# Kernel optimization log

Hardware: AMD Instinct MI355X
Metric: run time of the kernel (lower is better)

Reference implementation:

```python
import jax, jax.numpy as jnp
import numpy as np

VOCAB, EMBED, HIDDEN = 32000, 256, 512
N, L = 256, 512


def setup_inputs() -> dict:
    key = jax.random.key(0)
    ks = jax.random.split(key, 6)
    X = jax.random.randint(ks[0], (N, L), 0, VOCAB)
    emb = jax.random.normal(ks[1], (VOCAB, EMBED), dtype=jnp.float32)
    # torch Linear: y = x @ W.T + b, W:(out,in)
    W_hh = jax.random.normal(ks[2], (HIDDEN, HIDDEN), dtype=jnp.float32) / np.sqrt(HIDDEN)
    b_hh = jax.random.normal(ks[3], (HIDDEN,), dtype=jnp.float32) * 0.01
    W_xh = jax.random.normal(ks[4], (HIDDEN, EMBED), dtype=jnp.float32) / np.sqrt(EMBED)
    b_xh = jax.random.normal(ks[5], (HIDDEN,), dtype=jnp.float32) * 0.01
    return {"X": X, "emb": emb, "W_hh": W_hh, "b_hh": b_hh, "W_xh": W_xh, "b_xh": b_xh}


def reference(X, emb, W_hh, b_hh, W_xh, b_xh):
    Xe = emb[X]                       # (N, L, E) embedding lookup
    # precompute input projections for all steps (parallel GEMM)
    Xproj = jnp.einsum('nle,he->nlh', Xe, W_xh) + b_xh  # (N, L, H)
    Xproj_t = jnp.swapaxes(Xproj, 0, 1)                 # (L, N, H)
    h0 = jnp.zeros((X.shape[0], W_hh.shape[0]), dtype=emb.dtype)

    def step(h, xp):
        h_new = jnp.tanh(h @ W_hh.T + b_hh + xp)
        return h_new, None

    H_last, _ = jax.lax.scan(step, h0, Xproj_t)
    return H_last
```

## Files before the change

kernel.cpp:

```cpp
#include <hip/hip_runtime.h>


typedef _Float16 f16;
typedef f16 f16x8 __attribute__((ext_vector_type(8)));
typedef float f32x4 __attribute__((ext_vector_type(4)));
typedef unsigned short u16;

union U8 { uint4 u; f16x8 h; };
union U4 { uint2 u; f16 h[4]; };

__global__ void preconv_kernel(const float* __restrict__ W, u16* __restrict__ dst,
                               int kstride, int mode) {
  int t = blockIdx.x * blockDim.x + threadIdx.x;
  int f = t >> 6, l = t & 63;
  int kt, w, nt;
  if (mode == 0)    { kt = f & 7;  nt = (f >> 3) & 3; w = f >> 5; }
  else if (f < 384) { nt = f & 3;  w = (f >> 2) & 7;  kt = f >> 5; }
  else { int g = f - 384; kt = 12 + (g & 3); nt = (g >> 2) & 3; w = g >> 4; }
  int col = w * 64 + nt * 16 + (l & 15);
  int k   = kt * 32 + (l >> 4) * 8;
  const float* src = W + (size_t)col * kstride + k;
  float4 v0 = *(const float4*)src;
  float4 v1 = *(const float4*)(src + 4);
  U8 r;
  r.h = (f16x8){(f16)v0.x, (f16)v0.y, (f16)v0.z, (f16)v0.w,
                (f16)v1.x, (f16)v1.y, (f16)v1.z, (f16)v1.w};
  *(uint4*)(dst + (size_t)f * 512 + l * 8) = r.u;
}

__global__ __launch_bounds__(512, 2) void phaseA_kernel(
    const int* __restrict__ X, const float* __restrict__ emb,
    const u16* __restrict__ Wxf, const float* __restrict__ b_hh,
    const float* __restrict__ b_xh, u16* __restrict__ xpf) {
  __shared__ f16 A[128 * 256];
  const int tid = threadIdx.x, w = tid >> 6, l = tid & 63;
  const int b = blockIdx.x, bn = b >> 6, bl = b & 63;
  const int lr = l & 15, lg = l >> 4;

  f16x8 wx[4][8];
#pragma unroll
  for (int mt = 0; mt < 4; ++mt)
#pragma unroll
    for (int kt = 0; kt < 8; ++kt) {
      U8 u; u.u = *(const uint4*)(Wxf + (size_t)((w * 4 + mt) * 8 + kt) * 512 + l * 8);
      wx[mt][kt] = u.h;
    }
  float bias[4][4];
#pragma unroll
  for (int mt = 0; mt < 4; ++mt)
#pragma unroll
    for (int r = 0; r < 4; ++r) {
      int c = w * 64 + mt * 16 + lg * 4 + r;
      bias[mt][r] = b_hh[c] + b_xh[c];
    }

  int xs[16];
  const int lseq = bl * 8 + w;
#pragma unroll
  for (int i = 0; i < 16; ++i) xs[i] = X[(bn * 16 + i) * 512 + lseq];
#pragma unroll
  for (int i = 0; i < 16; ++i) {
    float4 v = *(const float4*)(emb + (size_t)xs[i] * 256 + l * 4);
    U4 p; p.h[0] = (f16)v.x; p.h[1] = (f16)v.y; p.h[2] = (f16)v.z; p.h[3] = (f16)v.w;
    int row = w * 16 + i;
    *(uint2*)(&A[row * 256 + ((l * 4) ^ ((row & 7) << 3))]) = p.u;
  }
  __syncthreads();

#pragma unroll 1
  for (int nt = 0; nt < 8; ++nt) {
    f32x4 acc[4];
#pragma unroll
    for (int mt = 0; mt < 4; ++mt) acc[mt] = (f32x4){0.f, 0.f, 0.f, 0.f};
    const f16* Brow = &A[(nt * 16 + lr) * 256];
    const int sw = (lr & 7) << 3;
#pragma unroll
    for (int kt = 0; kt < 8; ++kt) {
      f16x8 bfr = *(const f16x8*)(Brow + ((kt * 32 + lg * 8) ^ sw));
#pragma unroll
      for (int mt = 0; mt < 4; ++mt)
        acc[mt] = __builtin_amdgcn_mfma_f32_16x16x32_f16(wx[mt][kt], bfr, acc[mt], 0, 0, 0);
    }
    const int t = bl * 8 + nt;
#pragma unroll
    for (int mt = 0; mt < 4; ++mt) {
      U4 p;
#pragma unroll
      for (int r = 0; r < 4; ++r) p.h[r] = (f16)(acc[mt][r] + bias[mt][r]);
      *(uint2*)(xpf + (size_t)t * 131072 + (w * 16 + mt * 4 + lg) * 1024
                    + (bn * 16 + lr) * 4) = p.u;
    }
  }
}

__global__ __launch_bounds__(512)
__attribute__((amdgpu_waves_per_eu(2, 2)))
void phaseB_kernel(const u16* __restrict__ Whf, const u16* __restrict__ xpf,
                   float* __restrict__ out) {
  extern __shared__ char smem[];
  f16* h0 = (f16*)smem;
  f16* h1 = (f16*)(smem + 16 * 1024);
  u16* wl = (u16*)(smem + 32 * 1024);
  const int tid = threadIdx.x, w = tid >> 6, l = tid & 63;
  const int bb = blockIdx.x;
  const int lr = l & 15, lg = l >> 4;

  f16x8 wa[12][4];
#pragma unroll
  for (int kt = 0; kt < 12; ++kt)
#pragma unroll
    for (int mt = 0; mt < 4; ++mt) {
      U8 u; u.u = *(const uint4*)(Whf + (size_t)(kt * 32 + w * 4 + mt) * 512 + l * 8);
      wa[kt][mt] = u.h;
    }
  {
    const uint4* src = (const uint4*)(Whf + (size_t)384 * 512);
    uint4* dst = (uint4*)wl;
#pragma unroll
    for (int i = 0; i < 16; ++i) dst[i * 512 + tid] = src[i * 512 + tid];
  }
  {
    float* hz = (float*)h0;
#pragma unroll
    for (int i = 0; i < 8; ++i) hz[i * 512 + tid] = 0.f;
  }
  __syncthreads();

  const u16* wt  = wl + w * 8192 + l * 8;
  const u16* xpb = xpf + (w * 16 + lg) * 1024 + (bb * 16 + lr) * 4;
  const int asw = (lr & 7) << 3;

#define RNN_STEP(HR, HW, XP)                                                     \
  do {                                                                           \
    f32x4 acc[4];                                                                \
    _Pragma("unroll")                                                            \
    for (int mt = 0; mt < 4; ++mt) acc[mt] = (f32x4){0.f, 0.f, 0.f, 0.f};        \
    _Pragma("unroll")                                                            \
    for (int kt = 0; kt < 12; ++kt) {                                            \
      f16x8 hb = *(const f16x8*)((HR) + lr * 512 + ((kt * 32 + lg * 8) ^ asw));  \
      _Pragma("unroll")                                                          \
      for (int mt = 0; mt < 4; ++mt)                                             \
        acc[mt] = __builtin_amdgcn_mfma_f32_16x16x32_f16(wa[kt][mt], hb, acc[mt], 0, 0, 0); \
    }                                                                            \
    _Pragma("unroll")                                                            \
    for (int kt = 12; kt < 16; ++kt) {                                           \
      f16x8 hb = *(const f16x8*)((HR) + lr * 512 + ((kt * 32 + lg * 8) ^ asw));  \
      _Pragma("unroll")                                                          \
      for (int mt = 0; mt < 4; ++mt) {                                           \
        U8 u; u.u = *(const uint4*)(wt + (mt * 4 + (kt - 12)) * 512);            \
        acc[mt] = __builtin_amdgcn_mfma_f32_16x16x32_f16(u.h, hb, acc[mt], 0, 0, 0); \
      }                                                                          \
    }                                                                            \
    _Pragma("unroll")                                                            \
    for (int mt = 0; mt < 4; ++mt) {                                             \
      U4 px; px.u = (XP)[mt];                                                    \
      U4 o;                                                                      \
      _Pragma("unroll")                                                          \
      for (int r = 0; r < 4; ++r) {                                              \
        float z = acc[mt][r] + (float)px.h[r];                                   \
        float e = exp2f(z * 2.885390081777927f);                                 \
        o.h[r] = (f16)(1.0f - 2.0f * __builtin_amdgcn_rcpf(e + 1.0f));           \
      }                                                                          \
      *(uint2*)((HW) + lr * 512 + ((w * 64 + mt * 16 + lg * 4) ^ asw)) = o.u;    \
    }                                                                            \
    __syncthreads();                                                             \
  } while (0)

  uint2 xpA[4], xpB[4];
#pragma unroll
  for (int mt = 0; mt < 4; ++mt) xpA[mt] = *(const uint2*)(xpb + mt * 4096);

#pragma unroll 1
  for (int tt = 0; tt < 256; ++tt) {
    const int t = tt * 2;
    {
      const u16* p = xpb + (size_t)(t + 1) * 131072;
#pragma unroll
      for (int mt = 0; mt < 4; ++mt) xpB[mt] = *(const uint2*)(p + mt * 4096);
    }
    RNN_STEP(h0, h1, xpA);
    {
      const int tn = (t + 2 < 512) ? (t + 2) : 511;
      const u16* p = xpb + (size_t)tn * 131072;
#pragma unroll
      for (int mt = 0; mt < 4; ++mt) xpA[mt] = *(const uint2*)(p + mt * 4096);
    }
    RNN_STEP(h1, h0, xpB);
  }
#undef RNN_STEP

#pragma unroll
  for (int i = 0; i < 16; ++i) {
    f16 v = h0[i * 512 + (tid ^ ((i & 7) << 3))];
    out[(size_t)(bb * 16 + i) * 512 + tid] = (float)v;
  }
}

extern "C" void kernel_launch(void* const* d_in, const int* in_sizes, int n_in,
                              void* d_out, int out_size, void* d_ws, size_t ws_size,
                              hipStream_t stream) {
  const int*   X    = (const int*)d_in[0];
  const float* emb  = (const float*)d_in[1];
  const float* W_hh = (const float*)d_in[2];
  const float* b_hh = (const float*)d_in[3];
  const float* W_xh = (const float*)d_in[4];
  const float* b_xh = (const float*)d_in[5];
  float* out = (float*)d_out;

  char* ws = (char*)d_ws;
  u16* Whf = (u16*)ws;
  u16* Wxf = (u16*)(ws + 524288);
  u16* xpf = (u16*)(ws + 786432);

  hipFuncSetAttribute((const void*)phaseB_kernel,
                      hipFuncAttributeMaxDynamicSharedMemorySize, 163840);

  preconv_kernel<<<128, 256, 0, stream>>>(W_hh, Whf, 512, 1);
  preconv_kernel<<< 64, 256, 0, stream>>>(W_xh, Wxf, 256, 0);
  phaseA_kernel<<<1024, 512, 0, stream>>>(X, emb, Wxf, b_hh, b_xh, xpf);
  phaseB_kernel<<<16, 512, 163840, stream>>>(Whf, xpf, out);
}
```

Measured before the change: 1.104 ms.

## Split recurrent step across block pairs with flag-synchronized hidden-state exchange

Recurrence now runs on 32 blocks instead of 16. Each pair of blocks splits the 512 hidden outputs of a 16-row batch tile, and each block keeps its whole W_hh slice in registers instead of partly in LDS. Every step, a block publishes its half of h through global memory and spins on an acquire flag for its partner's half. The partner's half is only needed after the local-half MFMAs, so the wait can overlap with compute. This doubles the CUs used and removes LDS weight reads, but adds a global round-trip and cross-block sync on every step of the serial 512-step chain. The weight preconversion layout is changed to match.

```diff
diff --git a/kernel.cpp b/kernel.cpp
--- a/kernel.cpp
+++ b/kernel.cpp
@@ -13,11 +13,10 @@
                                int kstride, int mode) {
   int t = blockIdx.x * blockDim.x + threadIdx.x;
   int f = t >> 6, l = t & 63;
-  int kt, w, nt;
-  if (mode == 0)    { kt = f & 7;  nt = (f >> 3) & 3; w = f >> 5; }
-  else if (f < 384) { nt = f & 3;  w = (f >> 2) & 7;  kt = f >> 5; }
-  else { int g = f - 384; kt = 12 + (g & 3); nt = (g >> 2) & 3; w = g >> 4; }
-  int col = w * 64 + nt * 16 + (l & 15);
+  int kt, c16;
+  if (mode == 0) { kt = f & 7; c16 = f >> 3; }
+  else           { kt = f & 15; c16 = f >> 4; }
+  int col = c16 * 16 + (l & 15);
   int k   = kt * 32 + (l >> 4) * 8;
   const float* src = W + (size_t)col * kstride + k;
   float4 v0 = *(const float4*)src;
@@ -93,106 +92,124 @@
   }
 }
 
-__global__ __launch_bounds__(512)
-__attribute__((amdgpu_waves_per_eu(2, 2)))
-void phaseB_kernel(const u16* __restrict__ Whf, const u16* __restrict__ xpf,
-                   float* __restrict__ out) {
-  extern __shared__ char smem[];
-  f16* h0 = (f16*)smem;
-  f16* h1 = (f16*)(smem + 16 * 1024);
-  u16* wl = (u16*)(smem + 32 * 1024);
+__global__ __launch_bounds__(512, 2) void phaseB_kernel(
+    const u16* __restrict__ Whf, const u16* __restrict__ xpf,
+    u16* __restrict__ xch, int* __restrict__ flags, float* __restrict__ out) {
+  __shared__ f16 hb0[16][512];
+  __shared__ f16 hb1[16][512];
   const int tid = threadIdx.x, w = tid >> 6, l = tid & 63;
-  const int bb = blockIdx.x;
+  const int bb = blockIdx.x, pid = bb & 15, half = bb >> 4;
   const int lr = l & 15, lg = l >> 4;
-
-  f16x8 wa[12][4];
-#pragma unroll
-  for (int kt = 0; kt < 12; ++kt)
-#pragma unroll
-    for (int mt = 0; mt < 4; ++mt) {
-      U8 u; u.u = *(const uint4*)(Whf + (size_t)(kt * 32 + w * 4 + mt) * 512 + l * 8);
-      wa[kt][mt] = u.h;
-    }
+  const int asw = (lr & 7) << 3;
+  const int ownb = half * 256, othb = 256 - ownb;
+
+  f16x8 wreg[16][2];
+#pragma unroll
+  for (int i = 0; i < 16; ++i) {
+    const int ktg = (i < 8) ? (8 * half + i) : (8 * (1 - half) + (i - 8));
+#pragma unroll
+    for (int mt = 0; mt < 2; ++mt) {
+      const int f = (half * 16 + w * 2 + mt) * 16 + ktg;
+      U8 u; u.u = *(const uint4*)(Whf + (size_t)f * 512 + l * 8);
+      wreg[i][mt] = u.h;
+    }
+  }
   {
-    const uint4* src = (const uint4*)(Whf + (size_t)384 * 512);
-    uint4* dst = (uint4*)wl;
-#pragma unroll
-    for (int i = 0; i < 16; ++i) dst[i * 512 + tid] = src[i * 512 + tid];
-  }
-  {
-    float* hz = (float*)h0;
+    float* hz = (float*)hb0;
 #pragma unroll
     for (int i = 0; i < 8; ++i) hz[i * 512 + tid] = 0.f;
   }
   __syncthreads();
 
-  const u16* wt  = wl + w * 8192 + l * 8;
-  const u16* xpb = xpf + (w * 16 + lg) * 1024 + (bb * 16 + lr) * 4;
-  const int asw = (lr & 7) << 3;
-
-#define RNN_STEP(HR, HW, XP)                                                     \
-  do {                                                                           \
-    f32x4 acc[4];                                                                \
-    _Pragma("unroll")                                                            \
-    for (int mt = 0; mt < 4; ++mt) acc[mt] = (f32x4){0.f, 0.f, 0.f, 0.f};        \
-    _Pragma("unroll")                                                            \
-    for (int kt = 0; kt < 12; ++kt) {                                            \
-      f16x8 hb = *(const f16x8*)((HR) + lr * 512 + ((kt * 32 + lg * 8) ^ asw));  \
-      _Pragma("unroll")                                                          \
-      for (int mt = 0; mt < 4; ++mt)                                             \
-        acc[mt] = __builtin_amdgcn_mfma_f32_16x16x32_f16(wa[kt][mt], hb, acc[mt], 0, 0, 0); \
-    }                                                                            \
-    _Pragma("unroll")                                                            \
-    for (int kt = 12; kt < 16; ++kt) {                                           \
-      f16x8 hb = *(const f16x8*)((HR) + lr * 512 + ((kt * 32 + lg * 8) ^ asw));  \
-      _Pragma("unroll")                                                          \
-      for (int mt = 0; mt < 4; ++mt) {                                           \
-        U8 u; u.u = *(const uint4*)(wt + (mt * 4 + (kt - 12)) * 512);            \
-        acc[mt] = __builtin_amdgcn_mfma_f32_16x16x32_f16(u.h, hb, acc[mt], 0, 0, 0); \
-      }                                                                          \
-    }                                                                            \
-    _Pragma("unroll")                                                            \
-    for (int mt = 0; mt < 4; ++mt) {                                             \
-      U4 px; px.u = (XP)[mt];                                                    \
-      U4 o;                                                                      \
-      _Pragma("unroll")                                                          \
-      for (int r = 0; r < 4; ++r) {                                              \
-        float z = acc[mt][r] + (float)px.h[r];                                   \
-        float e = exp2f(z * 2.885390081777927f);                                 \
-        o.h[r] = (f16)(1.0f - 2.0f * __builtin_amdgcn_rcpf(e + 1.0f));           \
-      }                                                                          \
-      *(uint2*)((HW) + lr * 512 + ((w * 64 + mt * 16 + lg * 4) ^ asw)) = o.u;    \
-    }                                                                            \
-    __syncthreads();                                                             \
+  const u16* xpb = xpf + (size_t)(half * 64 + w * 8 + lg) * 1024 + (pid * 16 + lr) * 4;
+  int* const myflag = flags + pid * 2 + half;
+  int* const pflag  = flags + pid * 2 + (1 - half);
+  u16* const xo0 = xch + ((size_t)(0 * 16 + pid) * 2 + half) * 4096;
+  u16* const xo1 = xch + ((size_t)(1 * 16 + pid) * 2 + half) * 4096;
+  const u16* const xi0 = xch + ((size_t)(0 * 16 + pid) * 2 + (1 - half)) * 4096;
+  const u16* const xi1 = xch + ((size_t)(1 * 16 + pid) * 2 + (1 - half)) * 4096;
+  const int irow = tid >> 5, icol = othb + (tid & 31) * 8;
+  const int ioff = (irow * 512) + (icol ^ ((irow & 7) << 3));
+
+#define STEP(T, HC, HN, XPc, XPn, XIN, XOUT)                                      \
+  do {                                                                            \
+    {                          \
+      const int tn = ((T) + 1 < 512) ? ((T) + 1) : 511;                           \
+      const u16* p = xpb + (size_t)tn * 131072;                                   \
+      XPn[0] = *(const uint2*)(p);                                                \
+      XPn[1] = *(const uint2*)(p + 4096);                                         \
+    }                                                                             \
+    f32x4 acc0 = (f32x4){0.f, 0.f, 0.f, 0.f};                                     \
+    f32x4 acc1 = (f32x4){0.f, 0.f, 0.f, 0.f};                                     \
+    _Pragma("unroll")                                  \
+    for (int i = 0; i < 8; ++i) {                                                 \
+      f16x8 hf = *(const f16x8*)(&HC[lr][(ownb + i * 32 + lg * 8) ^ asw]);        \
+      acc0 = __builtin_amdgcn_mfma_f32_16x16x32_f16(wreg[i][0], hf, acc0, 0, 0, 0); \
+      acc1 = __builtin_amdgcn_mfma_f32_16x16x32_f16(wreg[i][1], hf, acc1, 0, 0, 0); \
+    }                                                                             \
+    if ((T) > 0) {                        \
+      int spins = 0;                                                              \
+      while (__hip_atomic_load(pflag, __ATOMIC_ACQUIRE,                           \
+                               __HIP_MEMORY_SCOPE_AGENT) < (T)) {                 \
+        if (++spins > (1 << 22)) break;                                           \
+      }                                                                           \
+      U8 v; v.u = *(const uint4*)(XIN + tid * 8);                                 \
+      *(uint4*)(&((f16*)HC)[ioff]) = v.u;                                         \
+    }                                                                             \
+    __syncthreads();                             \
+    _Pragma("unroll")                                   \
+    for (int i = 0; i < 8; ++i) {                                                 \
+      f16x8 hf = *(const f16x8*)(&HC[lr][(othb + i * 32 + lg * 8) ^ asw]);        \
+      acc0 = __builtin_amdgcn_mfma_f32_16x16x32_f16(wreg[8 + i][0], hf, acc0, 0, 0, 0); \
+      acc1 = __builtin_amdgcn_mfma_f32_16x16x32_f16(wreg[8 + i][1], hf, acc1, 0, 0, 0); \
+    }                                                                             \
+    {                             \
+      u16* xc = XOUT + lr * 256 + w * 32 + lg * 4;                                \
+      U4 px0; px0.u = XPc[0];                                                     \
+      U4 o0;                                                                      \
+      _Pragma("unroll")                                                           \
+      for (int r = 0; r < 4; ++r) {                                               \
+        float z = acc0[r] + (float)px0.h[r];                                      \
+        float e = exp2f(z * 2.885390081777927f);                                  \
+        o0.h[r] = (f16)(1.0f - 2.0f * __builtin_amdgcn_rcpf(e + 1.0f));           \
+      }                                                                           \
+      *(uint2*)(&HN[lr][(ownb + w * 32 + lg * 4) ^ asw]) = o0.u;                  \
+      *(uint2*)(xc) = o0.u;                                                       \
+      U4 px1; px1.u = XPc[1];                                                     \
+      U4 o1;                                                                      \
+      _Pragma("unroll")                                                           \
+      for (int r = 0; r < 4; ++r) {                                               \
+        float z = acc1[r] + (float)px1.h[r];                                      \
+        float e = exp2f(z * 2.885390081777927f);                                  \
+        o1.h[r] = (f16)(1.0f - 2.0f * __builtin_amdgcn_rcpf(e + 1.0f));           \
+      }                                                                           \
+      *(uint2*)(&HN[lr][(ownb + w * 32 + 16 + lg * 4) ^ asw]) = o1.u;             \
+      *(uint2*)(xc + 16) = o1.u;                                                  \
+    }                                                                             \
+    asm volatile("s_waitcnt vmcnt(0)" ::: "memory");    \
+    __syncthreads();                     \
+    if (tid == 0)                                                                 \
+      __hip_atomic_store(myflag, (T) + 1, __ATOMIC_RELEASE,                       \
+                         __HIP_MEMORY_SCOPE_AGENT);                               \
   } while (0)
 
-  uint2 xpA[4], xpB[4];
-#pragma unroll
-  for (int mt = 0; mt < 4; ++mt) xpA[mt] = *(const uint2*)(xpb + mt * 4096);
+  uint2 xpA[2], xpB[2];
+  xpA[0] = *(const uint2*)(xpb);
+  xpA[1] = *(const uint2*)(xpb + 4096);
 
 #pragma unroll 1
-  for (int tt = 0; tt < 256; ++tt) {
-    const int t = tt * 2;
-    {
-      const u16* p = xpb + (size_t)(t + 1) * 131072;
-#pragma unroll
-      for (int mt = 0; mt < 4; ++mt) xpB[mt] = *(const uint2*)(p + mt * 4096);
-    }
-    RNN_STEP(h0, h1, xpA);
-    {
-      const int tn = (t + 2 < 512) ? (t + 2) : 511;
-      const u16* p = xpb + (size_t)tn * 131072;
-#pragma unroll
-      for (int mt = 0; mt < 4; ++mt) xpA[mt] = *(const uint2*)(p + mt * 4096);
-    }
-    RNN_STEP(h1, h0, xpB);
-  }
-#undef RNN_STEP
-
-#pragma unroll
-  for (int i = 0; i < 16; ++i) {
-    f16 v = h0[i * 512 + (tid ^ ((i & 7) << 3))];
-    out[(size_t)(bb * 16 + i) * 512 + tid] = (float)v;
+  for (int t2 = 0; t2 < 256; ++t2) {
+    const int t = t2 * 2;
+    STEP(t,     hb0, hb1, xpA, xpB, xi0, xo1);
+    STEP(t + 1, hb1, hb0, xpB, xpA, xi1, xo0);
+  }
+#undef STEP
+
+#pragma unroll
+  for (int j = 0; j < 8; ++j) {
+    const int row = tid >> 5;
+    const int col = ownb + (tid & 31) * 8 + j;
+    out[(size_t)(pid * 16 + row) * 512 + col] = (float)hb0[row][col ^ ((row & 7) << 3)];
   }
 }
 
@@ -211,12 +228,16 @@
   u16* Whf = (u16*)ws;
   u16* Wxf = (u16*)(ws + 524288);
   u16* xpf = (u16*)(ws + 786432);
-
-  hipFuncSetAttribute((const void*)phaseB_kernel,
-                      hipFuncAttributeMaxDynamicSharedMemorySize, 163840);
+  u16* xch = (u16*)(ws + 786432 + 134217728);
+  int* flg = (int*)(ws + 786432 + 134217728 + 524288);
+
+  hipMemsetAsync(flg, 0, 32 * sizeof(int), stream);
 
   preconv_kernel<<<128, 256, 0, stream>>>(W_hh, Whf, 512, 1);
   preconv_kernel<<< 64, 256, 0, stream>>>(W_xh, Wxf, 256, 0);
   phaseA_kernel<<<1024, 512, 0, stream>>>(X, emb, Wxf, b_hh, b_xh, xpf);
-  phaseB_kernel<<<16, 512, 163840, stream>>>(Whf, xpf, out);
-}
+
+  void* args[] = {(void*)&Whf, (void*)&xpf, (void*)&xch, (void*)&flg, (void*)&out};
+  hipLaunchCooperativeKernel((void*)phaseB_kernel, dim3(32), dim3(512),
+                             args, 0, stream);
+}
```

After: 2.902 ms. 163% more time.

## Stream tail W_hh fragments from global/L2 instead of LDS, interleaved with MFMAs

Applied to the files above, without the earlier changes.

The recurrent kernel used to copy the last quarter of W_hh (the part that does not fit in registers) into LDS once and read it back every step. Now each step loads those fragments straight from global memory (L2-resident) in four batches, interleaved with the register-resident MFMA groups to hide latency. LDS shrinks to static hidden-state buffers only, and exp2f becomes the raw hardware builtin. The change trades LDS bandwidth and capacity for global/L2 latency on the serial critical path, which depends on the interleaving being enough to cover it.

```diff
diff --git a/kernel.cpp b/kernel.cpp
--- a/kernel.cpp
+++ b/kernel.cpp
@@ -93,17 +93,75 @@
   }
 }
 
+
+#define HFRAG(HR, KT) (*(const f16x8*)((HR) + lr * 512 + (((KT) * 32 + lg * 8) ^ asw)))
+
+#define MF_HEAD(HR, KT)                                                           \
+  do { f16x8 hf = HFRAG(HR, KT);                                                  \
+    _Pragma("unroll")                                                             \
+    for (int mt = 0; mt < 4; ++mt)                                                \
+      acc[mt] = __builtin_amdgcn_mfma_f32_16x16x32_f16(wa[KT][mt], hf, acc[mt], 0, 0, 0); \
+  } while (0)
+
+#define MF_TAIL(HR, KT, TT)                                                       \
+  do { f16x8 hf = HFRAG(HR, KT);                                                  \
+    _Pragma("unroll")                                                             \
+    for (int mt = 0; mt < 4; ++mt)                                                \
+      acc[mt] = __builtin_amdgcn_mfma_f32_16x16x32_f16(TT[mt].h, hf, acc[mt], 0, 0, 0); \
+  } while (0)
+
+#define TLOAD(TT, KOFF)                                                           \
+  do { _Pragma("unroll")                                                          \
+    for (int mt = 0; mt < 4; ++mt)                                                \
+      TT[mt].u = *(const uint4*)(gt + (size_t)(mt * 4 + (KOFF)) * 512);           \
+  } while (0)
+
+#define STEP(T, HR, HW, XPc, XPn)                                                 \
+  do {                                                                            \
+    {                          \
+      const int tn = ((T) + 1 < 512) ? ((T) + 1) : 511;                           \
+      const u16* p = xpb + (size_t)tn * 131072;                                   \
+      _Pragma("unroll")                                                           \
+      for (int mt = 0; mt < 4; ++mt) XPn[mt] = *(const uint2*)(p + mt * 4096);    \
+    }                                                                             \
+    f32x4 acc[4];                                                                 \
+    _Pragma("unroll")                                                             \
+    for (int mt = 0; mt < 4; ++mt) acc[mt] = (f32x4){0.f, 0.f, 0.f, 0.f};         \
+    U8 tA[4], tB[4], tC[4], tD[4];                                                \
+    TLOAD(tA, 0);                                                                 \
+    MF_HEAD(HR, 0); MF_HEAD(HR, 1); MF_HEAD(HR, 2); MF_HEAD(HR, 3);               \
+    TLOAD(tB, 1);                                                                 \
+    MF_HEAD(HR, 4); MF_HEAD(HR, 5); MF_HEAD(HR, 6); MF_HEAD(HR, 7);               \
+    TLOAD(tC, 2);                                                                 \
+    MF_HEAD(HR, 8); MF_HEAD(HR, 9); MF_HEAD(HR, 10); MF_HEAD(HR, 11);             \
+    TLOAD(tD, 3);                                                                 \
+    MF_TAIL(HR, 12, tA); MF_TAIL(HR, 13, tB);                                     \
+    MF_TAIL(HR, 14, tC); MF_TAIL(HR, 15, tD);                                     \
+    _Pragma("unroll")                                                             \
+    for (int mt = 0; mt < 4; ++mt) {                                              \
+      U4 px; px.u = XPc[mt];                                                      \
+      U4 o;                                                                       \
+      _Pragma("unroll")                                                           \
+      for (int r = 0; r < 4; ++r) {                                               \
+        float z = acc[mt][r] + (float)px.h[r];                                    \
+        float e = __builtin_amdgcn_exp2f(z * 2.885390081777927f);                 \
+        o.h[r] = (f16)(1.0f - 2.0f * __builtin_amdgcn_rcpf(e + 1.0f));            \
+      }                                                                           \
+      *(uint2*)((HW) + lr * 512 + ((w * 64 + mt * 16 + lg * 4) ^ asw)) = o.u;     \
+    }                                                                             \
+    __syncthreads();                                                              \
+  } while (0)
+
 __global__ __launch_bounds__(512)
 __attribute__((amdgpu_waves_per_eu(2, 2)))
 void phaseB_kernel(const u16* __restrict__ Whf, const u16* __restrict__ xpf,
                    float* __restrict__ out) {
-  extern __shared__ char smem[];
-  f16* h0 = (f16*)smem;
-  f16* h1 = (f16*)(smem + 16 * 1024);
-  u16* wl = (u16*)(smem + 32 * 1024);
+  __shared__ f16 hb0[16 * 512];
+  __shared__ f16 hb1[16 * 512];
   const int tid = threadIdx.x, w = tid >> 6, l = tid & 63;
   const int bb = blockIdx.x;
   const int lr = l & 15, lg = l >> 4;
+  const int asw = (lr & 7) << 3;
 
   f16x8 wa[12][4];
 #pragma unroll
@@ -114,87 +172,38 @@
       wa[kt][mt] = u.h;
     }
   {
-    const uint4* src = (const uint4*)(Whf + (size_t)384 * 512);
-    uint4* dst = (uint4*)wl;
-#pragma unroll
-    for (int i = 0; i < 16; ++i) dst[i * 512 + tid] = src[i * 512 + tid];
-  }
-  {
-    float* hz = (float*)h0;
+    float* hz = (float*)hb0;
 #pragma unroll
     for (int i = 0; i < 8; ++i) hz[i * 512 + tid] = 0.f;
   }
   __syncthreads();
 
-  const u16* wt  = wl + w * 8192 + l * 8;
-  const u16* xpb = xpf + (w * 16 + lg) * 1024 + (bb * 16 + lr) * 4;
-  const int asw = (lr & 7) << 3;
-
-#define RNN_STEP(HR, HW, XP)                                                     \
-  do {                                                                           \
-    f32x4 acc[4];                                                                \
-    _Pragma("unroll")                                                            \
-    for (int mt = 0; mt < 4; ++mt) acc[mt] = (f32x4){0.f, 0.f, 0.f, 0.f};        \
-    _Pragma("unroll")                                                            \
-    for (int kt = 0; kt < 12; ++kt) {                                            \
-      f16x8 hb = *(const f16x8*)((HR) + lr * 512 + ((kt * 32 + lg * 8) ^ asw));  \
-      _Pragma("unroll")                                                          \
-      for (int mt = 0; mt < 4; ++mt)                                             \
-        acc[mt] = __builtin_amdgcn_mfma_f32_16x16x32_f16(wa[kt][mt], hb, acc[mt], 0, 0, 0); \
-    }                                                                            \
-    _Pragma("unroll")                                                            \
-    for (int kt = 12; kt < 16; ++kt) {                                           \
-      f16x8 hb = *(const f16x8*)((HR) + lr * 512 + ((kt * 32 + lg * 8) ^ asw));  \
-      _Pragma("unroll")                                                          \
-      for (int mt = 0; mt < 4; ++mt) {                                           \
-        U8 u; u.u = *(const uint4*)(wt + (mt * 4 + (kt - 12)) * 512);            \
-        acc[mt] = __builtin_amdgcn_mfma_f32_16x16x32_f16(u.h, hb, acc[mt], 0, 0, 0); \
-      }                                                                          \
-    }                                                                            \
-    _Pragma("unroll")                                                            \
-    for (int mt = 0; mt < 4; ++mt) {                                             \
-      U4 px; px.u = (XP)[mt];                                                    \
-      U4 o;                                                                      \
-      _Pragma("unroll")                                                          \
-      for (int r = 0; r < 4; ++r) {                                              \
-        float z = acc[mt][r] + (float)px.h[r];                                   \
-        float e = exp2f(z * 2.885390081777927f);                                 \
-        o.h[r] = (f16)(1.0f - 2.0f * __builtin_amdgcn_rcpf(e + 1.0f));           \
-      }                                                                          \
-      *(uint2*)((HW) + lr * 512 + ((w * 64 + mt * 16 + lg * 4) ^ asw)) = o.u;    \
-    }                                                                            \
-    __syncthreads();                                                             \
-  } while (0)
+  const u16* gt  = Whf + (size_t)(384 + w * 16) * 512 + l * 8;
+  const u16* xpb = xpf + (size_t)(w * 16 + lg) * 1024 + (bb * 16 + lr) * 4;
 
   uint2 xpA[4], xpB[4];
 #pragma unroll
   for (int mt = 0; mt < 4; ++mt) xpA[mt] = *(const uint2*)(xpb + mt * 4096);
 
 #pragma unroll 1
-  for (int tt = 0; tt < 256; ++tt) {
-    const int t = tt * 2;
-    {
-      const u16* p = xpb + (size_t)(t + 1) * 131072;
-#pragma unroll
-      for (int mt = 0; mt < 4; ++mt) xpB[mt] = *(const uint2*)(p + mt * 4096);
-    }
-    RNN_STEP(h0, h1, xpA);
-    {
-      const int tn = (t + 2 < 512) ? (t + 2) : 511;
-      const u16* p = xpb + (size_t)tn * 131072;
-#pragma unroll
-      for (int mt = 0; mt < 4; ++mt) xpA[mt] = *(const uint2*)(p + mt * 4096);
-    }
-    RNN_STEP(h1, h0, xpB);
-  }
-#undef RNN_STEP
+  for (int t2 = 0; t2 < 256; ++t2) {
+    const int t = t2 * 2;
+    STEP(t,     hb0, hb1, xpA, xpB);
+    STEP(t + 1, hb1, hb0, xpB, xpA);
+  }
 
 #pragma unroll
   for (int i = 0; i < 16; ++i) {
-    f16 v = h0[i * 512 + (tid ^ ((i & 7) << 3))];
+    f16 v = hb0[i * 512 + (tid ^ ((i & 7) << 3))];
     out[(size_t)(bb * 16 + i) * 512 + tid] = (float)v;
   }
 }
+
+#undef STEP
+#undef TLOAD
+#undef MF_TAIL
+#undef MF_HEAD
+#undef HFRAG
 
 extern "C" void kernel_launch(void* const* d_in, const int* in_sizes, int n_in,
                               void* d_out, int out_size, void* d_ws, size_t ws_size,
@@ -212,11 +221,8 @@
   u16* Wxf = (u16*)(ws + 524288);
   u16* xpf = (u16*)(ws + 786432);
 
-  hipFuncSetAttribute((const void*)phaseB_kernel,
-                      hipFuncAttributeMaxDynamicSharedMemorySize, 163840);
-
   preconv_kernel<<<128, 256, 0, stream>>>(W_hh, Whf, 512, 1);
   preconv_kernel<<< 64, 256, 0, stream>>>(W_xh, Wxf, 256, 0);
   phaseA_kernel<<<1024, 512, 0, stream>>>(X, emb, Wxf, b_hh, b_xh, xpf);
-  phaseB_kernel<<<16, 512, 163840, stream>>>(Whf, xpf, out);
-}
+  phaseB_kernel<<<16, 512, 0, stream>>>(Whf, xpf, out);
+}
```

Measured after the change: 2.566 ms. 2.32x slower.
